# Kernel optimization log

Measured on AMD Instinct MI355X. Metric: run time of the kernel, lower is better.

## Reference

```python
import jax, jax.numpy as jnp
import numpy as np

K = 40          # neighbors, from __init__ default
EPS_BN = 1e-5   # BatchNorm eps; eval mode with running_mean=0, running_var=1


def knn_idx(x, k):
    # x: (B, C, N) -> indices (B, N, k) of k nearest neighbors (incl. self)
    xx = jnp.sum(x * x, axis=1)                      # (B, N)
    inner = jnp.einsum('bcn,bcm->bnm', x, x)         # (B, N, N)
    neg_dist = 2.0 * inner - xx[:, :, None] - xx[:, None, :]
    return jax.lax.top_k(neg_dist, k)[1]


def get_graph_feature(x, k):
    # DGCNN dynamic graph feature: (B, C, N) -> (B, 2C, N, k)
    idx = knn_idx(x, k)                              # (B, N, k) int
    xt = jnp.transpose(x, (0, 2, 1))                 # (B, N, C)
    nbr = jax.vmap(lambda f, i: f[i])(xt, idx)       # (B, N, k, C)
    ctr = xt[:, :, None, :]
    feat = jnp.concatenate([nbr - ctr, jnp.broadcast_to(ctr, nbr.shape)], axis=-1)
    return jnp.transpose(feat, (0, 3, 1, 2))         # (B, 2C, N, k)


def bn_affine(x, g, b, ch_axis=1):
    # eval-mode BatchNorm with running_mean=0, running_var=1
    shape = [1] * x.ndim
    shape[ch_axis] = -1
    scale = (g / jnp.sqrt(1.0 + EPS_BN)).reshape(shape)
    return x * scale + b.reshape(shape)


def conv_bn_lrelu2d(x, w, g, b):
    # 1x1 Conv2d (no bias) + BN2d + LeakyReLU(0.2); x: (B, Cin, N, k)
    y = jnp.einsum('oi,bink->bonk', w, x)
    return jax.nn.leaky_relu(bn_affine(y, g, b, 1), 0.2)


def sa_layer(x, qk, vw, vb, tw, tb, g, b):
    # PCT-style offset self-attention; q and k share weights. x: (B, C, N)
    xq = jnp.einsum('oc,bcn->bno', qk, x)            # (B, N, C/4)
    xk = jnp.einsum('oc,bcn->bon', qk, x)            # (B, C/4, N)
    xv = jnp.einsum('oc,bcn->bon', vw, x) + vb[None, :, None]
    energy = jnp.einsum('bno,bom->bnm', xq, xk)      # (B, N, N)
    attn = jax.nn.softmax(energy, axis=-1)
    attn = attn / (1e-9 + jnp.sum(attn, axis=1, keepdims=True))
    xr = jnp.einsum('bcn,bnm->bcm', xv, attn)        # (B, C, N)
    d = x - xr
    dr = jnp.einsum('oc,bcn->bon', tw, d) + tb[None, :, None]
    return x + jax.nn.relu(bn_affine(dr, g, b, 1))


def setup_inputs() -> dict:
    key = jax.random.key(0)
    ks = jax.random.split(key, 16)
    s = 0.05
    d = {
        'x': jax.random.normal(ks[0], (8, 2048, 3), jnp.float32),
        'w1': jax.random.normal(ks[1], (64, 6), jnp.float32) * s,
        'g1': jnp.ones((64,), jnp.float32), 'b1': jnp.zeros((64,), jnp.float32),
        'w2': jax.random.normal(ks[2], (64, 64), jnp.float32) * s,
        'g2': jnp.ones((64,), jnp.float32), 'b2': jnp.zeros((64,), jnp.float32),
        'w3': jax.random.normal(ks[3], (64, 128), jnp.float32) * s,
        'g3': jnp.ones((64,), jnp.float32), 'b3': jnp.zeros((64,), jnp.float32),
        'w4': jax.random.normal(ks[4], (64, 64), jnp.float32) * s,
        'g4': jnp.ones((64,), jnp.float32), 'b4': jnp.zeros((64,), jnp.float32),
        'w5': jax.random.normal(ks[5], (64, 128), jnp.float32) * s,
        'g5': jnp.ones((64,), jnp.float32), 'b5': jnp.zeros((64,), jnp.float32),
        'sa_qk': jax.random.normal(ks[6], (4, 32, 128), jnp.float32) * s,
        'sa_v': jax.random.normal(ks[7], (4, 128, 128), jnp.float32) * s,
        'sa_vb': jnp.zeros((4, 128), jnp.float32),
        'sa_t': jax.random.normal(ks[8], (4, 128, 128), jnp.float32) * s,
        'sa_tb': jnp.zeros((4, 128), jnp.float32),
        'sa_g': jnp.ones((4, 128), jnp.float32),
        'sa_b': jnp.zeros((4, 128), jnp.float32),
        'fuse_w': jax.random.normal(ks[9], (256, 512), jnp.float32) * s,
        'fuse_g': jnp.ones((256,), jnp.float32),
        'fuse_b': jnp.zeros((256,), jnp.float32),
    }
    return d


def reference(x, w1, g1, b1, w2, g2, b2, w3, g3, b3, w4, g4, b4, w5, g5, b5,
              sa_qk, sa_v, sa_vb, sa_t, sa_tb, sa_g, sa_b,
              fuse_w, fuse_g, fuse_b):
    xc = jnp.transpose(x, (0, 2, 1))                 # (B, 3, N)
    f = get_graph_feature(xc, K)                     # (B, 6, N, k)
    f = conv_bn_lrelu2d(f, w1, g1, b1)
    f = conv_bn_lrelu2d(f, w2, g2, b2)
    x1 = jnp.max(f, axis=-1)                         # (B, 64, N)
    f = get_graph_feature(x1, K)                     # (B, 128, N, k)
    f = conv_bn_lrelu2d(f, w3, g3, b3)
    f = conv_bn_lrelu2d(f, w4, g4, b4)
    x2 = jnp.max(f, axis=-1)                         # (B, 64, N)
    h = jnp.concatenate([x1, x2], axis=1)            # (B, 128, N)
    outs = []
    for i in range(4):
        h = sa_layer(h, sa_qk[i], sa_v[i], sa_vb[i], sa_t[i], sa_tb[i], sa_g[i], sa_b[i])
        outs.append(h)
    cat = jnp.concatenate(outs, axis=1)              # (B, 512, N)
    y = jnp.einsum('oi,bin->bon', fuse_w, cat)       # (B, 256, N)
    return jax.nn.leaky_relu(bn_affine(y, fuse_g, fuse_b, 1), 0.2)
```

## Files before the change

### kernel.cpp

```cpp
#include <hip/hip_runtime.h>

#define Bb 8
#define Nn 2048
#define Kk 40
#define HS (128*Nn)

__device__ __forceinline__ unsigned f2o(float f){
  unsigned u = __float_as_uint(f);
  return (u & 0x80000000u) ? ~u : (u | 0x80000000u);
}

__device__ __forceinline__ void wave_top40(float* d, int lane, int* op){
  float gv[4]; int gs[4];
  #pragma unroll
  for (int g=0; g<4; ++g){
    float bv = d[g*8]; int bs = g*8;
    #pragma unroll
    for (int j=1;j<8;++j){
      float v = d[g*8+j];
      if (v > bv){ bv = v; bs = g*8+j; }
    }
    gv[g]=bv; gs[g]=bs;
  }
  for (int t=0; t<Kk; ++t){
    float bv = gv[0]; int bs = gs[0];
    if (gv[1] > bv){ bv=gv[1]; bs=gs[1]; }
    if (gv[2] > bv){ bv=gv[2]; bs=gs[2]; }
    if (gv[3] > bv){ bv=gv[3]; bs=gs[3]; }
    int bm = bs*64 + lane;
    unsigned long long key = ((unsigned long long)f2o(bv) << 32) | (unsigned)(~bm);
    #pragma unroll
    for (int s=32;s>0;s>>=1){
      unsigned long long o = __shfl_xor(key, s, 64);
      if (o > key) key = o;
    }
    int wm = (int)(~(unsigned)key);
    if (lane == 0) op[t] = wm;
    bool mine = ((wm & 63) == lane);
    int wsl = wm >> 6;
    if (mine){
      int G = wsl >> 3;
      #pragma unroll
      for (int g=0; g<4; ++g){
        if (g == G){
          float nv = -__builtin_inff(); int ns = g*8;
          #pragma unroll
          for (int j=0;j<8;++j){
            float v = d[g*8+j];
            if (g*8+j == wsl) v = -__builtin_inff();
            d[g*8+j] = v;
            if (v > nv){ nv=v; ns=g*8+j; }
          }
          gv[g]=nv; gs[g]=ns;
        }
      }
    }
  }
}

__device__ __forceinline__ void wave_top40_g(float* d, int lane, int* op){
  float gv[4]; int gs[4];
  #pragma unroll
  for (int g=0; g<4; ++g){
    float bv = d[g*8]; int bs = g*8;
    #pragma unroll
    for (int j=1;j<8;++j){
      float v = d[g*8+j];
      if (v > bv){ bv = v; bs = g*8+j; }
    }
    gv[g]=bv; gs[g]=bs;
  }
  for (int t=0; t<Kk; ++t){
    float bv = gv[0]; int bs = gs[0];
    if (gv[1] > bv){ bv=gv[1]; bs=gs[1]; }
    if (gv[2] > bv){ bv=gv[2]; bs=gs[2]; }
    if (gv[3] > bv){ bv=gv[3]; bs=gs[3]; }
    int bm = ((bs>>2)<<8) + lane*4 + (bs&3);
    unsigned long long key = ((unsigned long long)f2o(bv) << 32) | (unsigned)(~bm);
    #pragma unroll
    for (int s=32;s>0;s>>=1){
      unsigned long long o = __shfl_xor(key, s, 64);
      if (o > key) key = o;
    }
    int wm = (int)(~(unsigned)key);
    if (lane == 0) op[t] = wm;
    bool mine = (((wm>>2) & 63) == lane);
    int wsl = ((wm>>8)<<2) | (wm & 3);
    if (mine){
      int G = wsl >> 3;
      #pragma unroll
      for (int g=0; g<4; ++g){
        if (g == G){
          float nv = -__builtin_inff(); int ns = g*8;
          #pragma unroll
          for (int j=0;j<8;++j){
            float v = d[g*8+j];
            if (g*8+j == wsl) v = -__builtin_inff();
            d[g*8+j] = v;
            if (v > nv){ nv=v; ns=g*8+j; }
          }
          gv[g]=nv; gs[g]=ns;
        }
      }
    }
  }
}

__global__ __launch_bounds__(256) void k_xx1(const float* __restrict__ x, float* __restrict__ XX){
  int e = blockIdx.x*256 + threadIdx.x;
  if (e >= Bb*Nn) return;
  float p0 = x[e*3+0], p1 = x[e*3+1], p2 = x[e*3+2];
  XX[e] = __fadd_rn(__fadd_rn(__fmul_rn(p0,p0), __fmul_rn(p1,p1)), __fmul_rn(p2,p2));
}

__global__ __launch_bounds__(256) void k_prep_wt(const float* __restrict__ w1, const float* __restrict__ w2,
                                                 const float* __restrict__ w3, const float* __restrict__ w4,
                                                 const float* __restrict__ fw,
                                                 float* __restrict__ W1T, float* __restrict__ W2T,
                                                 float* __restrict__ W3T, float* __restrict__ W4T,
                                                 float* __restrict__ FWT){
  int e = blockIdx.x*256 + threadIdx.x;
  if (e < 384)   { int i=e/64,  c=e%64;  W1T[e] = w1[c*6+i];    return; } e -= 384;
  if (e < 4096)  { int i=e/64,  c=e%64;  W2T[e] = w2[c*64+i];   return; } e -= 4096;
  if (e < 8192)  { int i=e/64,  c=e%64;  W3T[e] = w3[c*128+i];  return; } e -= 8192;
  if (e < 4096)  { int i=e/64,  c=e%64;  W4T[e] = w4[c*64+i];   return; } e -= 4096;
  if (e < 131072){ int i=e/256, o=e%256; FWT[e] = fw[o*512+i];  return; }
}

__global__ __launch_bounds__(256) void k_knn1(const float* __restrict__ P, const float* __restrict__ XX,
                                              int* __restrict__ IDX){
  int blk = blockIdx.x;
  int b = blk >> 9;
  int w = threadIdx.x >> 6, lane = threadIdx.x & 63;
  int n = (blk & 511)*4 + w;
  const float* Pb = P + b*Nn*3;
  const float* xb = XX + b*Nn;
  __shared__ float Pl[Nn*3];
  __shared__ float Xl[Nn];
  for (int e = threadIdx.x; e < Nn*3; e += 256) Pl[e] = Pb[e];
  for (int e = threadIdx.x; e < Nn; e += 256) Xl[e] = xb[e];
  __syncthreads();
  float c0 = Pl[n*3+0], c1 = Pl[n*3+1], c2 = Pl[n*3+2];
  float xn = Xl[n];
  float d[32];
  #pragma unroll
  for (int j=0;j<32;++j){
    int m = j*64 + lane;
    float a0 = Pl[m*3+0], a1 = Pl[m*3+1], a2 = Pl[m*3+2];
    float in_ = __fadd_rn(__fadd_rn(__fmul_rn(c0,a0), __fmul_rn(c1,a1)), __fmul_rn(c2,a2));
    d[j] = __fsub_rn(__fsub_rn(__fmul_rn(2.0f,in_), xn), Xl[m]);
  }
  wave_top40(d, lane, IDX + (b*Nn+n)*Kk);
}

__global__ __launch_bounds__(64) void k_ec1(const float* __restrict__ P, const int* __restrict__ IDX,
                                            const float* __restrict__ W1T, const float* __restrict__ W2T,
                                            const float* __restrict__ g1, const float* __restrict__ b1,
                                            const float* __restrict__ g2, const float* __restrict__ b2,
                                            float* __restrict__ X1T){
  int e = blockIdx.x;
  int b = e >> 11;
  int lane = threadIdx.x;
  __shared__ float dC[Kk*4];
  __shared__ __align__(16) float y1L[64*44];
  float c0 = P[e*3+0], c1 = P[e*3+1], c2 = P[e*3+2];
  if (lane < Kk) {
    int idx = IDX[e*Kk + lane] & (Nn-1);
    const float* pn = P + (b*Nn + idx)*3;
    dC[lane*4+0] = __fsub_rn(pn[0], c0);
    dC[lane*4+1] = __fsub_rn(pn[1], c1);
    dC[lane*4+2] = __fsub_rn(pn[2], c2);
  }
  __syncthreads();
  float w10 = W1T[0*64+lane], w11 = W1T[1*64+lane], w12 = W1T[2*64+lane];
  float w13 = W1T[3*64+lane], w14 = W1T[4*64+lane], w15 = W1T[5*64+lane];
  float p3 = __fmul_rn(w13,c0), p4 = __fmul_rn(w14,c1), p5 = __fmul_rn(w15,c2);
  float s1 = __fdiv_rn(g1[lane], __fsqrt_rn(1.0f + 1e-5f));
  float o1 = b1[lane];
  for (int k=0;k<Kk;++k){
    float t = __fmul_rn(w10, dC[k*4+0]);
    t = __fadd_rn(t, __fmul_rn(w11, dC[k*4+1]));
    t = __fadd_rn(t, __fmul_rn(w12, dC[k*4+2]));
    t = __fadd_rn(t, p3); t = __fadd_rn(t, p4); t = __fadd_rn(t, p5);
    float y = __fadd_rn(__fmul_rn(t, s1), o1);
    y = (y >= 0.0f) ? y : __fmul_rn(0.2f, y);
    y1L[lane*44+k] = y;
  }
  __syncthreads();
  float4 q[10];
  #pragma unroll
  for (int k4=0;k4<10;++k4) q[k4] = make_float4(0.f,0.f,0.f,0.f);
  for (int i=0;i<64;++i){
    float w = W2T[i*64+lane];
    const float4* yp = (const float4*)&y1L[i*44];
    #pragma unroll
    for (int k4=0;k4<10;++k4){
      float4 yv = yp[k4];
      q[k4].x = __fadd_rn(q[k4].x, __fmul_rn(w, yv.x));
      q[k4].y = __fadd_rn(q[k4].y, __fmul_rn(w, yv.y));
      q[k4].z = __fadd_rn(q[k4].z, __fmul_rn(w, yv.z));
      q[k4].w = __fadd_rn(q[k4].w, __fmul_rn(w, yv.w));
    }
  }
  float s2 = __fdiv_rn(g2[lane], __fsqrt_rn(1.0f + 1e-5f));
  float o2 = b2[lane];
  float mx = -__builtin_inff();
  #pragma unroll
  for (int k4=0;k4<10;++k4){
    float vs[4] = {q[k4].x, q[k4].y, q[k4].z, q[k4].w};
    #pragma unroll
    for (int j=0;j<4;++j){
      float y = __fadd_rn(__fmul_rn(vs[j], s2), o2);
      y = (y >= 0.0f) ? y : __fmul_rn(0.2f, y);
      mx = fmaxf(mx, y);
    }
  }
  X1T[e*64 + lane] = mx;
}

__global__ __launch_bounds__(256) void k_xx2(const float* __restrict__ X1T, float* __restrict__ XX2){
  int e = blockIdx.x*256 + threadIdx.x;
  const float* r = X1T + e*64;
  float a = 0.f;
  for (int c=0;c<64;++c) a = __fadd_rn(a, __fmul_rn(r[c], r[c]));
  XX2[e] = a;
}

__global__ __launch_bounds__(256) void k_knn2(const float* __restrict__ X1C, const float* __restrict__ XX2,
                                              int* __restrict__ IDX){
  int blk = blockIdx.x;
  int b = blk >> 9;
  int w = threadIdx.x >> 6, lane = threadIdx.x & 63;
  int n = (blk & 511)*4 + w;
  __shared__ float qL[4*64];
  { int t = threadIdx.x; int ww = t >> 6, c = t & 63;
    int nn = (blk & 511)*4 + ww;
    qL[t] = X1C[b*HS + c*Nn + nn]; }
  __syncthreads();
  const float* xb = XX2 + b*Nn;
  float4 a4[8];
  #pragma unroll
  for (int j=0;j<8;++j) a4[j] = make_float4(0.f,0.f,0.f,0.f);
  for (int c=0;c<64;++c){
    float qc = qL[w*64 + c];
    const float4* row = (const float4*)(X1C + b*HS + c*Nn);
    #pragma unroll
    for (int j=0;j<8;++j){
      float4 v = row[j*64 + lane];
      a4[j].x = __fadd_rn(a4[j].x, __fmul_rn(qc, v.x));
      a4[j].y = __fadd_rn(a4[j].y, __fmul_rn(qc, v.y));
      a4[j].z = __fadd_rn(a4[j].z, __fmul_rn(qc, v.z));
      a4[j].w = __fadd_rn(a4[j].w, __fmul_rn(qc, v.w));
    }
  }
  float xn = xb[n];
  float d[32];
  #pragma unroll
  for (int j=0;j<8;++j){
    float4 xm = ((const float4*)xb)[j*64 + lane];
    d[j*4+0] = __fsub_rn(__fsub_rn(__fmul_rn(2.0f, a4[j].x), xn), xm.x);
    d[j*4+1] = __fsub_rn(__fsub_rn(__fmul_rn(2.0f, a4[j].y), xn), xm.y);
    d[j*4+2] = __fsub_rn(__fsub_rn(__fmul_rn(2.0f, a4[j].z), xn), xm.z);
    d[j*4+3] = __fsub_rn(__fsub_rn(__fmul_rn(2.0f, a4[j].w), xn), xm.w);
  }
  wave_top40_g(d, lane, IDX + (b*Nn+n)*Kk);
}

__global__ __launch_bounds__(64) void k_ec2(const float* __restrict__ X1T, const int* __restrict__ IDX,
                                            const float* __restrict__ W3T, const float* __restrict__ W4T,
                                            const float* __restrict__ g3, const float* __restrict__ b3,
                                            const float* __restrict__ g4, const float* __restrict__ b4,
                                            float* __restrict__ X2T){
  int e = blockIdx.x; int b = e >> 11; int lane = threadIdx.x;
  __shared__ __align__(16) float dL[64*44];
  __shared__ float ctrL[64];
  float ctr = X1T[e*64 + lane];
  ctrL[lane] = ctr;
  __syncthreads();
  for (int k=0;k<Kk;++k){
    int idx = IDX[e*Kk + k] & (Nn-1);
    dL[lane*44 + k] = X1T[(b*Nn+idx)*64 + lane] - ctr;
  }
  __syncthreads();
  float base = 0.f;
  for (int i=0;i<64;++i) base = fmaf(W3T[(64+i)*64 + lane], ctrL[i], base);
  float4 q[10];
  #pragma unroll
  for (int k4=0;k4<10;++k4) q[k4] = make_float4(base,base,base,base);
  for (int i=0;i<64;++i){
    float w = W3T[i*64 + lane];
    const float4* dp = (const float4*)&dL[i*44];
    #pragma unroll
    for (int k4=0;k4<10;++k4){
      float4 d = dp[k4];
      q[k4].x = fmaf(w, d.x, q[k4].x);
      q[k4].y = fmaf(w, d.y, q[k4].y);
      q[k4].z = fmaf(w, d.z, q[k4].z);
      q[k4].w = fmaf(w, d.w, q[k4].w);
    }
  }
  float s3 = g3[lane] / sqrtf(1.0f+1e-5f);
  float o3 = b3[lane];
  __syncthreads();
  #pragma unroll
  for (int k4=0;k4<10;++k4){
    float4 y;
    y.x = q[k4].x*s3 + o3; y.x = (y.x>=0.f)?y.x:0.2f*y.x;
    y.y = q[k4].y*s3 + o3; y.y = (y.y>=0.f)?y.y:0.2f*y.y;
    y.z = q[k4].z*s3 + o3; y.z = (y.z>=0.f)?y.z:0.2f*y.z;
    y.w = q[k4].w*s3 + o3; y.w = (y.w>=0.f)?y.w:0.2f*y.w;
    *(float4*)&dL[lane*44 + k4*4] = y;
  }
  __syncthreads();
  float4 p[10];
  #pragma unroll
  for (int k4=0;k4<10;++k4) p[k4] = make_float4(0.f,0.f,0.f,0.f);
  for (int i=0;i<64;++i){
    float w = W4T[i*64 + lane];
    const float4* yp = (const float4*)&dL[i*44];
    #pragma unroll
    for (int k4=0;k4<10;++k4){
      float4 yv = yp[k4];
      p[k4].x = fmaf(w, yv.x, p[k4].x);
      p[k4].y = fmaf(w, yv.y, p[k4].y);
      p[k4].z = fmaf(w, yv.z, p[k4].z);
      p[k4].w = fmaf(w, yv.w, p[k4].w);
    }
  }
  float s4 = g4[lane] / sqrtf(1.0f+1e-5f);
  float o4 = b4[lane];
  float mx = -__builtin_inff();
  #pragma unroll
  for (int k4=0;k4<10;++k4){
    float vs[4] = {p[k4].x, p[k4].y, p[k4].z, p[k4].w};
    #pragma unroll
    for (int j=0;j<4;++j){
      float y = vs[j]*s4 + o4;
      y = (y>=0.f)?y:0.2f*y;
      mx = fmaxf(mx, y);
    }
  }
  X2T[e*64 + lane] = mx;
}

__global__ __launch_bounds__(256) void k_tr(const float* __restrict__ src, float* __restrict__ dst){
  int b = blockIdx.x >> 5; int n0 = (blockIdx.x & 31) << 6;
  __shared__ float t[64*65];
  for (int e=threadIdx.x; e<4096; e+=256){
    int r = e >> 6, c = e & 63;
    t[r*65+c] = src[(b*Nn + n0 + r)*64 + c];
  }
  __syncthreads();
  for (int e=threadIdx.x; e<4096; e+=256){
    int c = e >> 6, r = e & 63;
    dst[b*HS + c*Nn + n0 + r] = t[r*65+c];
  }
}

__global__ __launch_bounds__(256) void k_sa_a(const float* __restrict__ IN,
                                              const float* __restrict__ QKw, const float* __restrict__ Vw,
                                              const float* __restrict__ Vb,
                                              float* __restrict__ QX, float* __restrict__ XV){
  int blk = blockIdx.x;
  int part = blk & 1; int nt = (blk >> 1) & 31; int b = blk >> 6;
  int n0 = nt << 6;
  int w = threadIdx.x >> 6, lane = threadIdx.x & 63;
  __shared__ float xl[128*64];
  for (int e=threadIdx.x; e<8192; e+=256){
    int c = e >> 6, j = e & 63;
    xl[e] = IN[b*HS + c*Nn + n0 + j];
  }
  __syncthreads();
  for (int i=0;i<20;++i){
    int r = part*80 + w*20 + i;
    const float4* wp4;
    if (r < 32) wp4 = (const float4*)(QKw + r*128);
    else        wp4 = (const float4*)(Vw + (r-32)*128);
    float a = 0.f;
    #pragma unroll
    for (int c4=0;c4<32;++c4){
      float4 wv = wp4[c4];
      a = fmaf(wv.x, xl[(c4*4+0)*64 + lane], a);
      a = fmaf(wv.y, xl[(c4*4+1)*64 + lane], a);
      a = fmaf(wv.z, xl[(c4*4+2)*64 + lane], a);
      a = fmaf(wv.w, xl[(c4*4+3)*64 + lane], a);
    }
    if (r < 32) QX[(b*32+r)*Nn + n0 + lane] = a;
    else { int o = r-32; XV[(b*128+o)*Nn + n0 + lane] = a + Vb[o]; }
  }
}

__global__ __launch_bounds__(256) void k_sa_b(const float* __restrict__ QX,
                                              float* __restrict__ RMP, float* __restrict__ RSP){
  int blk = blockIdx.x;
  int b = blk >> 6, sub = blk & 63;
  int ncn = sub >> 3, mcn = sub & 7;
  int n = ncn*256 + threadIdx.x;
  float q[32];
  #pragma unroll
  for (int o=0;o<32;++o) q[o] = QX[(b*32+o)*Nn + n];
  __shared__ float qt[32*128];
  float mr = -__builtin_inff(), lr = 0.f;
  int m0 = mcn*256;
  for (int t=0;t<2;++t){
    for (int e=threadIdx.x; e<4096; e+=256){
      int o = e >> 7, mm = e & 127;
      qt[e] = QX[(b*32+o)*Nn + m0 + t*128 + mm];
    }
    __syncthreads();
    for (int mm=0;mm<128;mm+=2){
      float e0=0.f, e1=0.f;
      #pragma unroll
      for (int o=0;o<32;++o){ float qo=q[o]; e0=fmaf(qo, qt[o*128+mm], e0); e1=fmaf(qo, qt[o*128+mm+1], e1); }
      if (e0 > mr){ lr = lr*expf(mr-e0) + 1.f; mr = e0; } else lr += expf(e0-mr);
      if (e1 > mr){ lr = lr*expf(mr-e1) + 1.f; mr = e1; } else lr += expf(e1-mr);
    }
    __syncthreads();
  }
  RMP[(b*Nn+n)*8 + mcn] = mr;
  RSP[(b*Nn+n)*8 + mcn] = lr;
}

__global__ __launch_bounds__(256) void k_sa_b2(const float* __restrict__ RMP, const float* __restrict__ RSP,
                                               float* __restrict__ RMX, float* __restrict__ RSM){
  int e = blockIdx.x*256 + threadIdx.x;
  float M = -__builtin_inff();
  #pragma unroll
  for (int i=0;i<8;++i) M = fmaxf(M, RMP[e*8+i]);
  float l = 0.f;
  #pragma unroll
  for (int i=0;i<8;++i) l += RSP[e*8+i]*expf(RMP[e*8+i]-M);
  RMX[e] = M; RSM[e] = l;
}

#define SM_QM 0
#define SM_QN 1024
#define SM_XV 2048
#define SM_SL 6272
#define SM_MX 7296
#define SM_RL 7328

__global__ __launch_bounds__(256) void k_sa_cm(const float* __restrict__ QX, const float* __restrict__ XV,
                                               const float* __restrict__ RMAX, const float* __restrict__ RSUM,
                                               float* __restrict__ PP, float* __restrict__ CSP){
  int blk = blockIdx.x;
  int part = blk & 1, mt = (blk >> 1) & 63, b = blk >> 7;
  int m0 = mt << 5;
  int tid = threadIdx.x;
  int nnp = tid >> 4, mmp = tid & 15;
  int tc = tid >> 3, tm8 = tid & 7;
  __shared__ __align__(16) float sm[7360];
  for (int e=tid; e<1024; e+=256){
    int o = e >> 5, mm = e & 31;
    sm[SM_QM + e] = QX[(b*32+o)*Nn + m0 + mm];
  }
  float acc[4][4];
  #pragma unroll
  for (int ci=0;ci<4;++ci){
    #pragma unroll
    for (int mi=0;mi<4;++mi) acc[ci][mi] = 0.f;
  }
  float csr = 0.f;
  int it0 = part*32;
  for (int it=it0; it<it0+32; ++it){
    int nb = it*32;
    __syncthreads();
    for (int e=tid; e<1024; e+=256){ int o=e>>5, nn=e&31; sm[SM_QN+e] = QX[(b*32+o)*Nn + nb + nn]; }
    for (int e=tid; e<4096; e+=256){ int c=e>>5, nn=e&31; sm[SM_XV + nn*132 + c] = XV[(b*128+c)*Nn + nb + nn]; }
    if (tid < 32){ sm[SM_MX+tid] = RMAX[b*Nn + nb + tid]; sm[SM_RL+tid] = 1.0f / RSUM[b*Nn + nb + tid]; }
    __syncthreads();
    float e00=0.f, e01=0.f, e10=0.f, e11=0.f;
    #pragma unroll
    for (int o=0;o<32;++o){
      float2 qn = *(const float2*)&sm[SM_QN + o*32 + nnp*2];
      float2 qm = *(const float2*)&sm[SM_QM + o*32 + mmp*2];
      e00 = fmaf(qn.x, qm.x, e00);
      e01 = fmaf(qn.x, qm.y, e01);
      e10 = fmaf(qn.y, qm.x, e10);
      e11 = fmaf(qn.y, qm.y, e11);
    }
    float mx0 = sm[SM_MX + nnp*2],   rl0 = sm[SM_RL + nnp*2];
    float mx1 = sm[SM_MX + nnp*2+1], rl1 = sm[SM_RL + nnp*2+1];
    float2 s0; s0.x = expf(e00-mx0)*rl0; s0.y = expf(e01-mx0)*rl0;
    float2 s1; s1.x = expf(e10-mx1)*rl1; s1.y = expf(e11-mx1)*rl1;
    *(float2*)&sm[SM_SL + (nnp*2  )*32 + mmp*2] = s0;
    *(float2*)&sm[SM_SL + (nnp*2+1)*32 + mmp*2] = s1;
    __syncthreads();
    if (tid < 32){
      #pragma unroll
      for (int nn=0;nn<32;++nn) csr += sm[SM_SL + nn*32 + tid];
    }
    #pragma unroll 8
    for (int nn=0;nn<32;++nn){
      float4 xv4 = *(const float4*)&sm[SM_XV + nn*132 + tc*4];
      float4 s4  = *(const float4*)&sm[SM_SL + nn*32  + tm8*4];
      acc[0][0] = fmaf(xv4.x, s4.x, acc[0][0]);
      acc[0][1] = fmaf(xv4.x, s4.y, acc[0][1]);
      acc[0][2] = fmaf(xv4.x, s4.z, acc[0][2]);
      acc[0][3] = fmaf(xv4.x, s4.w, acc[0][3]);
      acc[1][0] = fmaf(xv4.y, s4.x, acc[1][0]);
      acc[1][1] = fmaf(xv4.y, s4.y, acc[1][1]);
      acc[1][2] = fmaf(xv4.y, s4.z, acc[1][2]);
      acc[1][3] = fmaf(xv4.y, s4.w, acc[1][3]);
      acc[2][0] = fmaf(xv4.z, s4.x, acc[2][0]);
      acc[2][1] = fmaf(xv4.z, s4.y, acc[2][1]);
      acc[2][2] = fmaf(xv4.z, s4.z, acc[2][2]);
      acc[2][3] = fmaf(xv4.z, s4.w, acc[2][3]);
      acc[3][0] = fmaf(xv4.w, s4.x, acc[3][0]);
      acc[3][1] = fmaf(xv4.w, s4.y, acc[3][1]);
      acc[3][2] = fmaf(xv4.w, s4.z, acc[3][2]);
      acc[3][3] = fmaf(xv4.w, s4.w, acc[3][3]);
    }
  }
  int slot = (b*64 + mt)*2 + part;
  #pragma unroll
  for (int ci=0;ci<4;++ci){
    int c = tc*4 + ci;
    *(float4*)&PP[slot*4096 + c*32 + tm8*4] =
      make_float4(acc[ci][0], acc[ci][1], acc[ci][2], acc[ci][3]);
  }
  if (tid < 32) CSP[slot*32 + tid] = csr;
}

__global__ __launch_bounds__(256) void k_sa_cc(const float* IN,
                                               const float* __restrict__ PP, const float* __restrict__ CSP,
                                               const float* __restrict__ Tw, const float* __restrict__ Tb,
                                               const float* __restrict__ Gs, const float* __restrict__ Bs,
                                               float* OUT){
  int blk = blockIdx.x;
  int mt = blk & 63, b = blk >> 6;
  int m0 = mt << 5;
  int tid = threadIdx.x;
  int tc = tid >> 3, tm8 = tid & 7;
  __shared__ __align__(16) float sm[4128];
  int s0 = (b*64 + mt)*2, s1 = s0 + 1;
  if (tid < 32) sm[4096 + tid] = CSP[s0*32 + tid] + CSP[s1*32 + tid];
  __syncthreads();
  #pragma unroll
  for (int ci=0;ci<4;++ci){
    int c = tc*4 + ci;
    float4 p0 = *(const float4*)&PP[s0*4096 + c*32 + tm8*4];
    float4 p1 = *(const float4*)&PP[s1*4096 + c*32 + tm8*4];
    float am[4] = {p0.x+p1.x, p0.y+p1.y, p0.z+p1.z, p0.w+p1.w};
    #pragma unroll
    for (int mi=0;mi<4;++mi){
      int ml = tm8*4 + mi;
      float cs = sm[4096 + ml];
      float xr = am[mi] / (1e-9f + cs);
      sm[c*32 + ml] = IN[b*HS + c*Nn + m0 + ml] - xr;
    }
  }
  __syncthreads();
  int hw = tid >> 5, m = tid & 31;
  float sroot = sqrtf(1.0f + 1e-5f);
  for (int oo=0; oo<16; ++oo){
    int o = oo*8 + hw;
    const float4* twp = (const float4*)(Tw + o*128);
    float a = 0.f;
    #pragma unroll
    for (int c4=0;c4<32;++c4){
      float4 wv = twp[c4];
      a = fmaf(wv.x, sm[(c4*4+0)*32 + m], a);
      a = fmaf(wv.y, sm[(c4*4+1)*32 + m], a);
      a = fmaf(wv.z, sm[(c4*4+2)*32 + m], a);
      a = fmaf(wv.w, sm[(c4*4+3)*32 + m], a);
    }
    a += Tb[o];
    float y = a * (Gs[o] / sroot) + Bs[o];
    y = fmaxf(y, 0.f);
    OUT[b*HS + o*Nn + m0 + m] = IN[b*HS + o*Nn + m0 + m] + y;
  }
}

__global__ __launch_bounds__(256) void k_fuse_part(const float* __restrict__ Hc, const float* __restrict__ FWT,
                                                   float* __restrict__ ACC, int l, int init, int fin,
                                                   const float* __restrict__ FGF, const float* __restrict__ FBF){
  int blk = blockIdx.x;
  int hf = blk & 1; int nt = (blk >> 1) & 31; int b = blk >> 6;
  int n0 = nt << 6;
  int w = threadIdx.x >> 6, lane = threadIdx.x & 63;
  __shared__ float xt[128*64];
  for (int e=threadIdx.x; e<8192; e+=256){
    int c = e >> 6, j = e & 63;
    xt[e] = Hc[(b*128 + c)*Nn + n0 + j];
  }
  __syncthreads();
  float4 a[8];
  #pragma unroll
  for (int j=0;j<8;++j) a[j] = make_float4(0.f,0.f,0.f,0.f);
  int ob = hf*128 + w*32;
  for (int c=0;c<128;++c){
    float xv = xt[c*64 + lane];
    const float4* wr = (const float4*)(FWT + (l*128+c)*256 + ob);
    #pragma unroll
    for (int j4=0;j4<8;++j4){
      float4 wv = wr[j4];
      a[j4].x = fmaf(wv.x, xv, a[j4].x);
      a[j4].y = fmaf(wv.y, xv, a[j4].y);
      a[j4].z = fmaf(wv.z, xv, a[j4].z);
      a[j4].w = fmaf(wv.w, xv, a[j4].w);
    }
  }
  float sroot = sqrtf(1.0f + 1e-5f);
  #pragma unroll
  for (int j4=0;j4<8;++j4){
    float vs[4] = {a[j4].x, a[j4].y, a[j4].z, a[j4].w};
    #pragma unroll
    for (int qq=0;qq<4;++qq){
      int o = ob + j4*4 + qq;
      int idx = (b*256 + o)*Nn + n0 + lane;
      float v = init ? vs[qq] : (ACC[idx] + vs[qq]);
      if (fin){
        float y = v * (FGF[o] / sroot) + FBF[o];
        y = (y >= 0.f) ? y : 0.2f*y;
        ACC[idx] = y;
      } else {
        ACC[idx] = v;
      }
    }
  }
}

extern "C" void kernel_launch(void* const* d_in, const int* in_sizes, int n_in,
                              void* d_out, int out_size, void* d_ws, size_t ws_size,
                              hipStream_t stream) {
  const float* X   = (const float*)d_in[0];
  const float* w1  = (const float*)d_in[1];
  const float* g1  = (const float*)d_in[2];
  const float* b1  = (const float*)d_in[3];
  const float* w2  = (const float*)d_in[4];
  const float* g2  = (const float*)d_in[5];
  const float* b2_ = (const float*)d_in[6];
  const float* w3  = (const float*)d_in[7];
  const float* g3  = (const float*)d_in[8];
  const float* b3  = (const float*)d_in[9];
  const float* w4  = (const float*)d_in[10];
  const float* g4  = (const float*)d_in[11];
  const float* b4  = (const float*)d_in[12];
  const float* qk  = (const float*)d_in[16];
  const float* sv  = (const float*)d_in[17];
  const float* svb = (const float*)d_in[18];
  const float* st  = (const float*)d_in[19];
  const float* stb = (const float*)d_in[20];
  const float* sg  = (const float*)d_in[21];
  const float* sb  = (const float*)d_in[22];
  const float* fw  = (const float*)d_in[23];
  const float* fg  = (const float*)d_in[24];
  const float* fb  = (const float*)d_in[25];

  float* ws = (float*)d_ws;
  float* H    = ws + 0;
  float* QXb  = ws + 2097152;
  float* XVb  = ws + 2621440;
  float* RMP  = ws + 4718592;
  float* RSP  = ws + 4849664;
  float* RMX  = ws + 4980736;
  float* RSM  = ws + 4997120;
  float* XX   = ws + 2146304;
  int*   IDX  = (int*)(ws + 2162688);
  float* X1T  = ws + 2818048;
  float* X2T  = ws + 3866624;
  float* C0   = ws + 5013504;
  float* W1T = C0 + 0;
  float* W2T = C0 + 384;
  float* W3T = C0 + 4480;
  float* W4T = C0 + 12672;
  float* FWT = C0 + 16768;
  float* PP  = ws + 5161344;
  float* CSP = ws + 9355648;
  float* ACC = (float*)d_out;

  k_xx1<<<64,256,0,stream>>>(X, XX);
  k_prep_wt<<<578,256,0,stream>>>(w1,w2,w3,w4,fw, W1T,W2T,W3T,W4T,FWT);
  k_knn1<<<4096,256,0,stream>>>(X, XX, IDX);
  k_ec1<<<16384,64,0,stream>>>(X, IDX, W1T, W2T, g1,b1,g2,b2_, X1T);
  k_xx2<<<64,256,0,stream>>>(X1T, XX);
  k_tr<<<256,256,0,stream>>>(X1T, H);
  k_knn2<<<4096,256,0,stream>>>(H, XX, IDX);
  k_ec2<<<16384,64,0,stream>>>(X1T, IDX, W3T, W4T, g3,b3,g4,b4, X2T);
  k_tr<<<256,256,0,stream>>>(X2T, H + 64*Nn);

  for (int l=0;l<4;++l){
    k_sa_a<<<512,256,0,stream>>>(H, qk + l*4096, sv + l*16384, svb + l*128, QXb, XVb);
    k_sa_b<<<512,256,0,stream>>>(QXb, RMP, RSP);
    k_sa_b2<<<64,256,0,stream>>>(RMP, RSP, RMX, RSM);
    k_sa_cm<<<1024,256,0,stream>>>(QXb, XVb, RMX, RSM, PP, CSP);
    k_sa_cc<<<512,256,0,stream>>>(H, PP, CSP,
                                  st + l*16384, stb + l*128, sg + l*128, sb + l*128, H);
    k_fuse_part<<<512,256,0,stream>>>(H, FWT, ACC, l, (l==0)?1:0, (l==3)?1:0, fg, fb);
  }
}
```

Before: 2.681 ms.

## Tile knn2 distance computation: 16 queries per block with LDS-staged candidate rows

Rewrites the second kNN kernel so each block handles 16 query points (4 per wave) instead of 4, staging candidate feature chunks in shared memory and reusing each loaded value across 4 queries per wave. This cuts global/L2 reads of the candidate matrix roughly fourfold. In exchange each thread holds 128 accumulator floats plus 40KB of LDS per block, which raises register pressure, lowers occupancy and shrinks the grid to 1024 blocks.

```diff
diff --git a/kernel.cpp b/kernel.cpp
--- a/kernel.cpp
+++ b/kernel.cpp
@@ -229,41 +229,65 @@
 __global__ __launch_bounds__(256) void k_knn2(const float* __restrict__ X1C, const float* __restrict__ XX2,
                                               int* __restrict__ IDX){
   int blk = blockIdx.x;
-  int b = blk >> 9;
+  int b = blk >> 7;
+  int n0 = (blk & 127) << 4;
   int w = threadIdx.x >> 6, lane = threadIdx.x & 63;
-  int n = (blk & 511)*4 + w;
-  __shared__ float qL[4*64];
-  { int t = threadIdx.x; int ww = t >> 6, c = t & 63;
-    int nn = (blk & 511)*4 + ww;
-    qL[t] = X1C[b*HS + c*Nn + nn]; }
-  __syncthreads();
+  __shared__ __align__(16) float buf[4*2048];
+  __shared__ __align__(16) float qL[64*16];
+  for (int e=threadIdx.x; e<1024; e+=256){
+    int c = e >> 4, t = e & 15;
+    qL[e] = X1C[b*HS + c*Nn + n0 + t];
+  }
+  float4 acc[4][8];
+  #pragma unroll
+  for (int qi=0;qi<4;++qi){
+    #pragma unroll
+    for (int j=0;j<8;++j) acc[qi][j] = make_float4(0.f,0.f,0.f,0.f);
+  }
+  const float4* src4 = (const float4*)(X1C + b*HS);
+  float4* buf4 = (float4*)buf;
+#define KNN2_ACC(Q, QS) \
+    acc[Q][j].x = __fadd_rn(acc[Q][j].x, __fmul_rn(QS, v.x)); \
+    acc[Q][j].y = __fadd_rn(acc[Q][j].y, __fmul_rn(QS, v.y)); \
+    acc[Q][j].z = __fadd_rn(acc[Q][j].z, __fmul_rn(QS, v.z)); \
+    acc[Q][j].w = __fadd_rn(acc[Q][j].w, __fmul_rn(QS, v.w));
+  for (int cc=0; cc<16; ++cc){
+    __syncthreads();
+    #pragma unroll
+    for (int e=0;e<8;++e)
+      buf4[e*256 + threadIdx.x] = src4[cc*2048 + e*256 + threadIdx.x];
+    __syncthreads();
+    #pragma unroll
+    for (int c4=0;c4<4;++c4){
+      float4 q = *(const float4*)&qL[(cc*4+c4)*16 + w*4];
+      #pragma unroll
+      for (int j=0;j<8;++j){
+        float4 v = buf4[c4*512 + j*64 + lane];
+        KNN2_ACC(0, q.x)
+        KNN2_ACC(1, q.y)
+        KNN2_ACC(2, q.z)
+        KNN2_ACC(3, q.w)
+      }
+    }
+  }
+#undef KNN2_ACC
   const float* xb = XX2 + b*Nn;
-  float4 a4[8];
-  #pragma unroll
-  for (int j=0;j<8;++j) a4[j] = make_float4(0.f,0.f,0.f,0.f);
-  for (int c=0;c<64;++c){
-    float qc = qL[w*64 + c];
-    const float4* row = (const float4*)(X1C + b*HS + c*Nn);
+  const float4* xb4 = (const float4*)xb;
+  #pragma unroll
+  for (int qi=0;qi<4;++qi){
+    int n = n0 + w*4 + qi;
+    float xn = xb[n];
+    float d[32];
     #pragma unroll
     for (int j=0;j<8;++j){
-      float4 v = row[j*64 + lane];
-      a4[j].x = __fadd_rn(a4[j].x, __fmul_rn(qc, v.x));
-      a4[j].y = __fadd_rn(a4[j].y, __fmul_rn(qc, v.y));
-      a4[j].z = __fadd_rn(a4[j].z, __fmul_rn(qc, v.z));
-      a4[j].w = __fadd_rn(a4[j].w, __fmul_rn(qc, v.w));
-    }
-  }
-  float xn = xb[n];
-  float d[32];
-  #pragma unroll
-  for (int j=0;j<8;++j){
-    float4 xm = ((const float4*)xb)[j*64 + lane];
-    d[j*4+0] = __fsub_rn(__fsub_rn(__fmul_rn(2.0f, a4[j].x), xn), xm.x);
-    d[j*4+1] = __fsub_rn(__fsub_rn(__fmul_rn(2.0f, a4[j].y), xn), xm.y);
-    d[j*4+2] = __fsub_rn(__fsub_rn(__fmul_rn(2.0f, a4[j].z), xn), xm.z);
-    d[j*4+3] = __fsub_rn(__fsub_rn(__fmul_rn(2.0f, a4[j].w), xn), xm.w);
-  }
-  wave_top40_g(d, lane, IDX + (b*Nn+n)*Kk);
+      float4 xm = xb4[j*64 + lane];
+      d[j*4+0] = __fsub_rn(__fsub_rn(__fmul_rn(2.0f, acc[qi][j].x), xn), xm.x);
+      d[j*4+1] = __fsub_rn(__fsub_rn(__fmul_rn(2.0f, acc[qi][j].y), xn), xm.y);
+      d[j*4+2] = __fsub_rn(__fsub_rn(__fmul_rn(2.0f, acc[qi][j].z), xn), xm.z);
+      d[j*4+3] = __fsub_rn(__fsub_rn(__fmul_rn(2.0f, acc[qi][j].w), xn), xm.w);
+    }
+    wave_top40_g(d, lane, IDX + (b*Nn + n)*Kk);
+  }
 }
 
 __global__ __launch_bounds__(64) void k_ec2(const float* __restrict__ X1T, const int* __restrict__ IDX,
@@ -676,7 +700,7 @@
   k_ec1<<<16384,64,0,stream>>>(X, IDX, W1T, W2T, g1,b1,g2,b2_, X1T);
   k_xx2<<<64,256,0,stream>>>(X1T, XX);
   k_tr<<<256,256,0,stream>>>(X1T, H);
-  k_knn2<<<4096,256,0,stream>>>(H, XX, IDX);
+  k_knn2<<<1024,256,0,stream>>>(H, XX, IDX);
   k_ec2<<<16384,64,0,stream>>>(X1T, IDX, W3T, W4T, g3,b3,g4,b4, X2T);
   k_tr<<<256,256,0,stream>>>(X2T, H + 64*Nn);
 
```

New measurement: 2.970 ms. 1.11x slower.
